# Kernel optimization log

Measured on AMD Instinct MI355X. Metric: run time of the kernel, lower is better.

## Reference

```python
import jax, jax.numpy as jnp
import numpy as np

QK = 32  # GGML Q8_0 block size

def dequant_q8_0(w_q, w_scales):
    # w_q: [out, in] int8-valued quants; w_scales: [out, in//QK] per-block scales
    out_f, in_f = w_q.shape
    q = w_q.astype(w_scales.dtype).reshape(out_f, in_f // QK, QK)
    w = q * w_scales[:, :, None]  # broadcast scale over block
    return w.reshape(out_f, in_f)

def setup_inputs() -> dict:
    key = jax.random.key(0)
    k1, k2, k3, k4 = jax.random.split(key, 4)
    OUT, IN, TOK = 12288, 3072, 4096
    x = jax.random.normal(k1, (TOK, IN), dtype=jnp.float32)
    w_q = jax.random.randint(k2, (OUT, IN), -127, 128, dtype=jnp.int32)
    w_scales = jax.random.uniform(k3, (OUT, IN // QK), dtype=jnp.float32) * 0.01
    bias = jax.random.normal(k4, (OUT,), dtype=jnp.float32) * 0.01
    return {"x": x, "w_q": w_q, "w_scales": w_scales, "bias": bias}

def reference(x, w_q, w_scales, bias):
    # DequantingLinear.forward: dequantize weight (and bias) then F.linear
    weight = dequant_q8_0(w_q, w_scales)          # [OUT, IN]
    return x @ weight.T + bias                    # [TOK, OUT]
```

## Files before the change

### kernel.cpp

```cpp
#include <hip/hip_runtime.h>
#include <hip/hip_bf16.h>
#include <stdint.h>


typedef __bf16 bf16;
typedef __bf16 bf16x8 __attribute__((ext_vector_type(8)));
typedef float f32x4 __attribute__((ext_vector_type(4)));

#define AS1 __attribute__((address_space(1)))
#define AS3 __attribute__((address_space(3)))

__device__ __forceinline__ void gload_lds16(const void* g, void* l) {
    __builtin_amdgcn_global_load_lds((AS1 void*)g, (AS3 void*)l, 16, 0, 0);
}

#define MFMA16(d, x, y) d = __builtin_amdgcn_mfma_f32_16x16x32_bf16(x, y, d, 0, 0, 0)

__global__ __launch_bounds__(128) void k_dequant(
    const int* __restrict__ q, const float* __restrict__ sc,
    bf16* __restrict__ w, int IN) {
    const int row = blockIdx.y;
    const int k = (blockIdx.x * 128 + threadIdx.x) * 8;
    if (k >= IN) return;
    const float s = sc[(size_t)row * (IN >> 5) + (k >> 5)];
    const size_t base = (size_t)row * IN + k;
    const int4 q0 = *(const int4*)(q + base);
    const int4 q1 = *(const int4*)(q + base + 4);
    bf16x8 o;
    o[0] = (bf16)(q0.x * s); o[1] = (bf16)(q0.y * s);
    o[2] = (bf16)(q0.z * s); o[3] = (bf16)(q0.w * s);
    o[4] = (bf16)(q1.x * s); o[5] = (bf16)(q1.y * s);
    o[6] = (bf16)(q1.z * s); o[7] = (bf16)(q1.w * s);
    *(bf16x8*)(w + base) = o;
}

__global__ __launch_bounds__(256) void k_cvt(
    const float* __restrict__ x, bf16* __restrict__ xb, long long n8) {
    long long i = (long long)blockIdx.x * 256 + threadIdx.x;
    const long long stride = (long long)gridDim.x * 256;
    for (; i < n8; i += stride) {
        const float4 a = *(const float4*)(x + i * 8);
        const float4 b = *(const float4*)(x + i * 8 + 4);
        bf16x8 o;
        o[0] = (bf16)a.x; o[1] = (bf16)a.y; o[2] = (bf16)a.z; o[3] = (bf16)a.w;
        o[4] = (bf16)b.x; o[5] = (bf16)b.y; o[6] = (bf16)b.z; o[7] = (bf16)b.w;
        *(bf16x8*)(xb + i * 8) = o;
    }
}

__global__ __launch_bounds__(512, 2) void k_gemm8p(
    const bf16* __restrict__ A, const bf16* __restrict__ B,
    const float* __restrict__ bias, float* __restrict__ C,
    int M, int N, int K) {
    __shared__ __align__(16) char lds[131072];
    const int tid = threadIdx.x;
    const int wv = tid >> 6, ln = tid & 63;
    const int wm = wv >> 2, wn = wv & 3;
    const int nbn = N >> 8;
    const int nwg = gridDim.x;
    const int q8 = nwg >> 3, r8 = nwg & 7;
    const int xcd = blockIdx.x & 7, lin = blockIdx.x >> 3;
    const int swz = (xcd < r8 ? xcd * (q8 + 1)
                              : r8 * (q8 + 1) + (xcd - r8) * q8) + lin;
    const int bm = swz / nbn, bn = swz % nbn;

    const size_t rowb = (size_t)K * 2;
    const int scol = (((tid ^ (tid >> 3)) & 7) << 4);
    const char* Ag = (const char*)A + ((size_t)(bm << 8) + (tid >> 3)) * rowb + scol;
    const char* Bg = (const char*)B + ((size_t)(bn << 8) + (tid >> 3)) * rowb + scol;
    const char* Ag128 = Ag + (size_t)128 * rowb;
    const char* Bg128 = Bg + (size_t)128 * rowb;
    const int ldsw = wv << 10;

#define STG(dst_, src_, kt_) do {                                             \
        const size_t kb_ = (size_t)(kt_) << 1;                                \
        gload_lds16((src_) + kb_, lds + (dst_) + ldsw);                       \
        gload_lds16((src_) + (size_t)64 * rowb + kb_,                         \
                    lds + (dst_) + 8192 + ldsw);                              \
    } while (0)

    const int colx = ((ln & 4) << 4) | ((((ln >> 4) ^ ln) & 3) << 4);
    const int c0 = colx, c1 = colx ^ 64;
    const int abase = (((wm << 7) + (ln & 15)) << 7);
    const int bbase = (((wn << 6) + (ln & 15)) << 7);

    f32x4 acc[8][4] = {};

#define SB __builtin_amdgcn_sched_barrier(0)
#define BAR __builtin_amdgcn_s_barrier()
#define VMW2 asm volatile("s_waitcnt vmcnt(2)" ::: "memory")
#define VMW0 asm volatile("s_waitcnt vmcnt(0)" ::: "memory")

#define PHASE(cb_, h_, c_, STAGE_STMT, ENDW_STMT) do {                        \
        const char* bA_ = lds + (cb_);                                        \
        const char* bB_ = lds + (cb_) + 32768;                                \
        bf16x8 paf[8], pbf[4];                                                \
        _Pragma("unroll")                                                     \
        for (int r = 0; r < 4; ++r) {                                         \
            paf[r*2+0] = *(const bf16x8*)(bA_ + abase + (h_)*8192 + (r<<11) + c0); \
            paf[r*2+1] = *(const bf16x8*)(bA_ + abase + (h_)*8192 + (r<<11) + c1); \
        }                                                                     \
        _Pragma("unroll")                                                     \
        for (int rb = 0; rb < 2; ++rb) {                                      \
            pbf[rb*2+0] = *(const bf16x8*)(bB_ + bbase + (((c_)*2+rb)<<11) + c0); \
            pbf[rb*2+1] = *(const bf16x8*)(bB_ + bbase + (((c_)*2+rb)<<11) + c1); \
        }                                                                     \
        STAGE_STMT;                                                           \
        SB; BAR; SB;                                                          \
        __builtin_amdgcn_s_setprio(1);                                        \
        _Pragma("unroll")                                                     \
        for (int r = 0; r < 4; ++r)                                           \
            _Pragma("unroll")                                                 \
            for (int rb = 0; rb < 2; ++rb) {                                  \
                MFMA16(acc[(h_)*4+r][(c_)*2+rb], paf[r*2+0], pbf[rb*2+0]);    \
                MFMA16(acc[(h_)*4+r][(c_)*2+rb], paf[r*2+1], pbf[rb*2+1]);    \
            }                                                                 \
        __builtin_amdgcn_s_setprio(0);                                        \
        ENDW_STMT;                                                            \
        SB; BAR; SB;                                                          \
    } while (0)

    STG(0,      Ag,    0);
    STG(16384,  Ag128, 0);
    STG(32768,  Bg,    0);
    STG(49152,  Bg128, 0);
    STG(65536,  Ag,    64);
    VMW2;
    SB; BAR; SB;

    const int NITER = K >> 7;
    for (int j = 0; j < NITER - 1; ++j) {
        const int kt1 = (j << 7) + 64, kt2 = kt1 + 64, kt3 = kt2 + 64;
        PHASE(0,     0, 0, STG(81920,  Ag128, kt1), (void)0);
        PHASE(0,     0, 1, STG(98304,  Bg,    kt1), (void)0);
        PHASE(0,     1, 0, STG(114688, Bg128, kt1), (void)0);
        PHASE(0,     1, 1, STG(0,      Ag,    kt2), VMW2);
        PHASE(65536, 0, 0, STG(16384,  Ag128, kt2), (void)0);
        PHASE(65536, 0, 1, STG(32768,  Bg,    kt2), (void)0);
        PHASE(65536, 1, 0, STG(49152,  Bg128, kt2), (void)0);
        PHASE(65536, 1, 1, STG(65536,  Ag,    kt3), VMW2);
    }
    {
        const int kt1 = ((NITER - 1) << 7) + 64;
        PHASE(0,     0, 0, STG(81920,  Ag128, kt1), (void)0);
        PHASE(0,     0, 1, STG(98304,  Bg,    kt1), (void)0);
        PHASE(0,     1, 0, STG(114688, Bg128, kt1), (void)0);
        PHASE(0,     1, 1, (void)0,                 VMW0);
        PHASE(65536, 0, 0, (void)0, (void)0);
        PHASE(65536, 0, 1, (void)0, (void)0);
        PHASE(65536, 1, 0, (void)0, (void)0);
        PHASE(65536, 1, 1, (void)0, (void)0);
    }
#undef PHASE
#undef STG

    const int erow = (bm << 8) + (wm << 7) + ((ln >> 4) << 2);
    const int ecol = (bn << 8) + (wn << 6) + (ln & 15);
    float bv[4];
#pragma unroll
    for (int n = 0; n < 4; ++n) bv[n] = bias[ecol + (n << 4)];
#pragma unroll
    for (int m = 0; m < 8; ++m)
#pragma unroll
        for (int r = 0; r < 4; ++r) {
            float* Crow = C + (size_t)(erow + (m << 4) + r) * N + ecol;
#pragma unroll
            for (int n = 0; n < 4; ++n)
                Crow[n << 4] = acc[m][n][r] + bv[n];
        }
}

__global__ __launch_bounds__(256) void k_fused(
    const float* __restrict__ X, const int* __restrict__ Q,
    const float* __restrict__ SC, const float* __restrict__ bias,
    float* __restrict__ C, int M, int N, int K) {
    __shared__ __align__(16) bf16 sA[128 * 32];
    __shared__ __align__(16) bf16 sB[128 * 32];
    const int tid = threadIdx.x;
    const int wv = tid >> 6;
    const int ln = tid & 63;
    const int nbn = N >> 7;
    const int nwg = gridDim.x;
    const int q8 = nwg >> 3, r8 = nwg & 7;
    const int xcd = blockIdx.x & 7, lin = blockIdx.x >> 3;
    const int swz = (xcd < r8 ? xcd * (q8 + 1)
                              : r8 * (q8 + 1) + (xcd - r8) * q8) + lin;
    const int bm = swz / nbn, bn = swz % nbn;
    const int wr = (wv >> 1) << 6;
    const int wc = (wv & 1) << 6;
    const int srow = tid >> 1;
    const int sk = (tid & 1) << 4;

    f32x4 acc[4][4] = {};
    const float* xrow = X + (size_t)((bm << 7) + srow) * K + sk;
    const int* qrow = Q + (size_t)((bn << 7) + srow) * K + sk;
    const float* scrow = SC + (size_t)((bn << 7) + srow) * (K >> 5);

    for (int kt = 0; kt < K; kt += 32) {
        const float4 a0 = *(const float4*)(xrow + kt);
        const float4 a1 = *(const float4*)(xrow + kt + 4);
        const float4 a2 = *(const float4*)(xrow + kt + 8);
        const float4 a3 = *(const float4*)(xrow + kt + 12);
        const int4 q0 = *(const int4*)(qrow + kt);
        const int4 q1 = *(const int4*)(qrow + kt + 4);
        const int4 q2 = *(const int4*)(qrow + kt + 8);
        const int4 q3 = *(const int4*)(qrow + kt + 12);
        const float s = scrow[(kt + sk) >> 5];
        bf16x8 wa0, wa1, wb0, wb1;
        wa0[0] = (bf16)a0.x; wa0[1] = (bf16)a0.y; wa0[2] = (bf16)a0.z; wa0[3] = (bf16)a0.w;
        wa0[4] = (bf16)a1.x; wa0[5] = (bf16)a1.y; wa0[6] = (bf16)a1.z; wa0[7] = (bf16)a1.w;
        wa1[0] = (bf16)a2.x; wa1[1] = (bf16)a2.y; wa1[2] = (bf16)a2.z; wa1[3] = (bf16)a2.w;
        wa1[4] = (bf16)a3.x; wa1[5] = (bf16)a3.y; wa1[6] = (bf16)a3.z; wa1[7] = (bf16)a3.w;
        wb0[0] = (bf16)(q0.x * s); wb0[1] = (bf16)(q0.y * s);
        wb0[2] = (bf16)(q0.z * s); wb0[3] = (bf16)(q0.w * s);
        wb0[4] = (bf16)(q1.x * s); wb0[5] = (bf16)(q1.y * s);
        wb0[6] = (bf16)(q1.z * s); wb0[7] = (bf16)(q1.w * s);
        wb1[0] = (bf16)(q2.x * s); wb1[1] = (bf16)(q2.y * s);
        wb1[2] = (bf16)(q2.z * s); wb1[3] = (bf16)(q2.w * s);
        wb1[4] = (bf16)(q3.x * s); wb1[5] = (bf16)(q3.y * s);
        wb1[6] = (bf16)(q3.z * s); wb1[7] = (bf16)(q3.w * s);
        __syncthreads();
        *(bf16x8*)(sA + srow * 32 + sk) = wa0;
        *(bf16x8*)(sA + srow * 32 + sk + 8) = wa1;
        *(bf16x8*)(sB + srow * 32 + sk) = wb0;
        *(bf16x8*)(sB + srow * 32 + sk + 8) = wb1;
        __syncthreads();

        bf16x8 af[4], bg[4];
#pragma unroll
        for (int m = 0; m < 4; ++m)
            af[m] = *(const bf16x8*)(sA + ((wr + (m << 4) + (ln & 15)) << 5) +
                                     ((ln >> 4) << 3));
#pragma unroll
        for (int n = 0; n < 4; ++n)
            bg[n] = *(const bf16x8*)(sB + ((wc + (n << 4) + (ln & 15)) << 5) +
                                     ((ln >> 4) << 3));
#pragma unroll
        for (int m = 0; m < 4; ++m)
#pragma unroll
            for (int n = 0; n < 4; ++n)
                acc[m][n] = __builtin_amdgcn_mfma_f32_16x16x32_bf16(
                    af[m], bg[n], acc[m][n], 0, 0, 0);
    }

    float bv[4];
#pragma unroll
    for (int n = 0; n < 4; ++n)
        bv[n] = bias[(bn << 7) + wc + (n << 4) + (ln & 15)];
#pragma unroll
    for (int m = 0; m < 4; ++m) {
        const int grow0 = (bm << 7) + wr + (m << 4) + ((ln >> 4) << 2);
#pragma unroll
        for (int r = 0; r < 4; ++r) {
            float* Crow = C + (size_t)(grow0 + r) * N;
#pragma unroll
            for (int n = 0; n < 4; ++n)
                Crow[(bn << 7) + wc + (n << 4) + (ln & 15)] =
                    acc[m][n][r] + bv[n];
        }
    }
}

extern "C" void kernel_launch(void* const* d_in, const int* in_sizes, int n_in,
                              void* d_out, int out_size, void* d_ws, size_t ws_size,
                              hipStream_t stream) {
    const float* x = (const float*)d_in[0];
    const int* wq = (const int*)d_in[1];
    const float* sc = (const float*)d_in[2];
    const float* bias = (const float*)d_in[3];
    float* out = (float*)d_out;

    const long long xN = in_sizes[0];
    const long long wN = in_sizes[1];
    const int OUT = in_sizes[3];
    const int IN = (int)(wN / OUT);
    const int TOK = (int)(xN / IN);
    const int M = TOK, N = OUT, K = IN;

    const size_t wb_bytes = (size_t)wN * 2;
    const size_t xb_bytes = (size_t)xN * 2;
    const bool ok8p = (M % 256 == 0) && (N % 256 == 0) && (K % 128 == 0) &&
                      (K >= 256);

    if (ok8p && ws_size >= wb_bytes + xb_bytes) {
        bf16* Wb = (bf16*)d_ws;
        bf16* Xb = (bf16*)((char*)d_ws + wb_bytes);
        dim3 dq_grid((IN / 8 + 127) / 128, OUT);
        k_dequant<<<dq_grid, 128, 0, stream>>>(wq, sc, Wb, IN);
        const long long n8 = xN / 8;
        int cvt_blocks = (int)((n8 + 255) / 256);
        if (cvt_blocks > 2048) cvt_blocks = 2048;
        k_cvt<<<cvt_blocks, 256, 0, stream>>>(x, Xb, n8);
        const int grid = (M / 256) * (N / 256);
        k_gemm8p<<<grid, 512, 0, stream>>>(Xb, Wb, bias, out, M, N, K);
    } else {
        const int grid = (M / 128) * (N / 128);
        k_fused<<<grid, 256, 0, stream>>>(x, wq, sc, bias, out, M, N, K);
    }
}
```

Baseline: 361.0 us.

## Restructure GEMM LDS staging into per-quadrant A/B loads with finer waits

Reorganizes the 8-phase bf16 MFMA GEMM pipeline so each phase stages one quadrant of A or B into the other double buffer. The previous one-stage-ahead ring offset is replaced by a plain two-buffer ping-pong. The B tile rows are remapped so each staged quadrant matches the column half consumed by a phase. Each phase now has one barrier plus a vmcnt(4) wait where the old code had two barriers per phase and vmcnt(2) waits. The aim is to reduce barrier overhead and keep more global loads in flight, at the cost of relying on subtle wait-count correctness. The K>=256 guard is also dropped.

```diff
diff --git a/kernel.cpp b/kernel.cpp
--- a/kernel.cpp
+++ b/kernel.cpp
@@ -67,46 +67,55 @@
     const size_t rowb = (size_t)K * 2;
     const int scol = (((tid ^ (tid >> 3)) & 7) << 4);
     const char* Ag = (const char*)A + ((size_t)(bm << 8) + (tid >> 3)) * rowb + scol;
-    const char* Bg = (const char*)B + ((size_t)(bn << 8) + (tid >> 3)) * rowb + scol;
-    const char* Ag128 = Ag + (size_t)128 * rowb;
-    const char* Bg128 = Bg + (size_t)128 * rowb;
+    const char* Bg = (const char*)B +
+        ((size_t)(bn << 8) + ((tid >> 8) << 6) + ((tid >> 3) & 31)) * rowb + scol;
     const int ldsw = wv << 10;
 
-#define STG(dst_, src_, kt_) do {                                             \
+#define STGA(bb_, h_, kt_) do {                                               \
         const size_t kb_ = (size_t)(kt_) << 1;                                \
-        gload_lds16((src_) + kb_, lds + (dst_) + ldsw);                       \
-        gload_lds16((src_) + (size_t)64 * rowb + kb_,                         \
-                    lds + (dst_) + 8192 + ldsw);                              \
+        gload_lds16(Ag + (size_t)((h_) << 6) * rowb + kb_,                    \
+                    lds + (bb_) + ((h_) << 14) + ldsw);                       \
+        gload_lds16(Ag + (size_t)(128 + ((h_) << 6)) * rowb + kb_,            \
+                    lds + (bb_) + ((h_) << 14) + 8192 + ldsw);                \
+    } while (0)
+#define STGB(bb_, c_, kt_) do {                                               \
+        const size_t kb_ = (size_t)(kt_) << 1;                                \
+        gload_lds16(Bg + (size_t)((c_) << 5) * rowb + kb_,                    \
+                    lds + (bb_) + 32768 + ((c_) << 14) + ldsw);               \
+        gload_lds16(Bg + (size_t)(128 + ((c_) << 5)) * rowb + kb_,            \
+                    lds + (bb_) + 32768 + ((c_) << 14) + 8192 + ldsw);        \
     } while (0)
 
     const int colx = ((ln & 4) << 4) | ((((ln >> 4) ^ ln) & 3) << 4);
     const int c0 = colx, c1 = colx ^ 64;
-    const int abase = (((wm << 7) + (ln & 15)) << 7);
-    const int bbase = (((wn << 6) + (ln & 15)) << 7);
+    const int arow = (wm << 13) + ((ln & 15) << 7);
+    const int brow = (wn << 12) + ((ln & 15) << 7);
 
     f32x4 acc[8][4] = {};
 
 #define SB __builtin_amdgcn_sched_barrier(0)
 #define BAR __builtin_amdgcn_s_barrier()
-#define VMW2 asm volatile("s_waitcnt vmcnt(2)" ::: "memory")
-#define VMW0 asm volatile("s_waitcnt vmcnt(0)" ::: "memory")
-
-#define PHASE(cb_, h_, c_, STAGE_STMT, ENDW_STMT) do {                        \
-        const char* bA_ = lds + (cb_);                                        \
-        const char* bB_ = lds + (cb_) + 32768;                                \
+#define EW4 do { asm volatile("s_waitcnt vmcnt(4)" ::: "memory"); SB; BAR; SB; } while (0)
+#define EW2 do { asm volatile("s_waitcnt vmcnt(2)" ::: "memory"); SB; BAR; SB; } while (0)
+#define EW0 do { asm volatile("s_waitcnt vmcnt(0)" ::: "memory"); SB; BAR; SB; } while (0)
+#define EWN do { BAR; SB; } while (0)
+
+#define PHASE(bb_, h_, c_, STAGE_STMT, ENDW_STMT) do {                        \
+        const char* uA_ = lds + (bb_) + ((h_) << 14);                         \
+        const char* uB_ = lds + (bb_) + 32768 + ((c_) << 14);                 \
         bf16x8 paf[8], pbf[4];                                                \
         _Pragma("unroll")                                                     \
         for (int r = 0; r < 4; ++r) {                                         \
-            paf[r*2+0] = *(const bf16x8*)(bA_ + abase + (h_)*8192 + (r<<11) + c0); \
-            paf[r*2+1] = *(const bf16x8*)(bA_ + abase + (h_)*8192 + (r<<11) + c1); \
+            paf[r*2+0] = *(const bf16x8*)(uA_ + arow + (r << 11) + c0);       \
+            paf[r*2+1] = *(const bf16x8*)(uA_ + arow + (r << 11) + c1);       \
         }                                                                     \
         _Pragma("unroll")                                                     \
         for (int rb = 0; rb < 2; ++rb) {                                      \
-            pbf[rb*2+0] = *(const bf16x8*)(bB_ + bbase + (((c_)*2+rb)<<11) + c0); \
-            pbf[rb*2+1] = *(const bf16x8*)(bB_ + bbase + (((c_)*2+rb)<<11) + c1); \
+            pbf[rb*2+0] = *(const bf16x8*)(uB_ + brow + (rb << 11) + c0);     \
+            pbf[rb*2+1] = *(const bf16x8*)(uB_ + brow + (rb << 11) + c1);     \
         }                                                                     \
         STAGE_STMT;                                                           \
-        SB; BAR; SB;                                                          \
+        BAR;                                                                  \
         __builtin_amdgcn_s_setprio(1);                                        \
         _Pragma("unroll")                                                     \
         for (int r = 0; r < 4; ++r)                                           \
@@ -117,42 +126,41 @@
             }                                                                 \
         __builtin_amdgcn_s_setprio(0);                                        \
         ENDW_STMT;                                                            \
-        SB; BAR; SB;                                                          \
     } while (0)
 
-    STG(0,      Ag,    0);
-    STG(16384,  Ag128, 0);
-    STG(32768,  Bg,    0);
-    STG(49152,  Bg128, 0);
-    STG(65536,  Ag,    64);
-    VMW2;
-    SB; BAR; SB;
+    STGA(0, 0, 0);
+    STGB(0, 0, 0);
+    STGB(0, 1, 0);
+    STGA(0, 1, 0);
+    EW4;
 
     const int NITER = K >> 7;
     for (int j = 0; j < NITER - 1; ++j) {
-        const int kt1 = (j << 7) + 64, kt2 = kt1 + 64, kt3 = kt2 + 64;
-        PHASE(0,     0, 0, STG(81920,  Ag128, kt1), (void)0);
-        PHASE(0,     0, 1, STG(98304,  Bg,    kt1), (void)0);
-        PHASE(0,     1, 0, STG(114688, Bg128, kt1), (void)0);
-        PHASE(0,     1, 1, STG(0,      Ag,    kt2), VMW2);
-        PHASE(65536, 0, 0, STG(16384,  Ag128, kt2), (void)0);
-        PHASE(65536, 0, 1, STG(32768,  Bg,    kt2), (void)0);
-        PHASE(65536, 1, 0, STG(49152,  Bg128, kt2), (void)0);
-        PHASE(65536, 1, 1, STG(65536,  Ag,    kt3), VMW2);
+        const int ko = (j << 7) + 64;
+        const int kn = (j << 7) + 128;
+        PHASE(0,     0, 0, STGA(65536, 0, ko), EW4);
+        PHASE(0,     0, 1, STGB(65536, 0, ko), EW4);
+        PHASE(0,     1, 1, STGB(65536, 1, ko), EWN);
+        PHASE(0,     1, 0, STGA(65536, 1, ko), EW4);
+        PHASE(65536, 0, 0, STGA(0, 0, kn),     EW4);
+        PHASE(65536, 0, 1, STGB(0, 0, kn),     EW4);
+        PHASE(65536, 1, 1, STGB(0, 1, kn),     EWN);
+        PHASE(65536, 1, 0, STGA(0, 1, kn),     EW4);
     }
     {
-        const int kt1 = ((NITER - 1) << 7) + 64;
-        PHASE(0,     0, 0, STG(81920,  Ag128, kt1), (void)0);
-        PHASE(0,     0, 1, STG(98304,  Bg,    kt1), (void)0);
-        PHASE(0,     1, 0, STG(114688, Bg128, kt1), (void)0);
-        PHASE(0,     1, 1, (void)0,                 VMW0);
-        PHASE(65536, 0, 0, (void)0, (void)0);
-        PHASE(65536, 0, 1, (void)0, (void)0);
-        PHASE(65536, 1, 0, (void)0, (void)0);
-        PHASE(65536, 1, 1, (void)0, (void)0);
+        const int ko = ((NITER - 1) << 7) + 64;
+        PHASE(0,     0, 0, STGA(65536, 0, ko), EW4);
+        PHASE(0,     0, 1, STGB(65536, 0, ko), EW4);
+        PHASE(0,     1, 1, STGB(65536, 1, ko), EWN);
+        PHASE(0,     1, 0, STGA(65536, 1, ko), EW4);
+        PHASE(65536, 0, 0, (void)0,            EW2);
+        PHASE(65536, 0, 1, (void)0,            EW0);
+        PHASE(65536, 1, 1, (void)0,            EWN);
+        PHASE(65536, 1, 0, (void)0,            EWN);
     }
 #undef PHASE
-#undef STG
+#undef STGA
+#undef STGB
 
     const int erow = (bm << 8) + (wm << 7) + ((ln >> 4) << 2);
     const int ecol = (bn << 8) + (wn << 6) + (ln & 15);
@@ -279,8 +287,7 @@
 
     const size_t wb_bytes = (size_t)wN * 2;
     const size_t xb_bytes = (size_t)xN * 2;
-    const bool ok8p = (M % 256 == 0) && (N % 256 == 0) && (K % 128 == 0) &&
-                      (K >= 256);
+    const bool ok8p = (M % 256 == 0) && (N % 256 == 0) && (K % 128 == 0);
 
     if (ok8p && ws_size >= wb_bytes + xb_bytes) {
         bf16* Wb = (bf16*)d_ws;
```

Measured after the change: 361.9 us. No clear change (+0.2%).

## Reuse LDS fragments across MFMA clusters with serpentine order and reworked staging

Applied to the files above, without the earlier changes.

Reorders the 8-phase GEMM main loop into a serpentine cluster order (h0c0, h0c1, h1c1, h1c0) so A and B register fragments read from LDS are reused across consecutive MFMA clusters instead of reloaded every phase. This cuts LDS read traffic per K-step. The global-to-LDS staging schedule and buffer slot assignments are also reworked, with the waitcnt changed to vmcnt(4) and the sched_barrier hints removed. The changes add register pressure from keeping two B fragment sets live, and they risk new hazards in the reworked LDS buffer reuse ordering.

```diff
diff --git a/kernel.cpp b/kernel.cpp
--- a/kernel.cpp
+++ b/kernel.cpp
@@ -65,94 +65,101 @@
     const int bm = swz / nbn, bn = swz % nbn;
 
     const size_t rowb = (size_t)K * 2;
+    const size_t r64 = (size_t)64 * rowb, r128 = (size_t)128 * rowb;
     const int scol = (((tid ^ (tid >> 3)) & 7) << 4);
     const char* Ag = (const char*)A + ((size_t)(bm << 8) + (tid >> 3)) * rowb + scol;
     const char* Bg = (const char*)B + ((size_t)(bn << 8) + (tid >> 3)) * rowb + scol;
-    const char* Ag128 = Ag + (size_t)128 * rowb;
-    const char* Bg128 = Bg + (size_t)128 * rowb;
+    const char* Ah = Ag + r128;
+    const char* Bh = Bg + r128;
     const int ldsw = wv << 10;
 
-#define STG(dst_, src_, kt_) do {                                             \
+#define STGU(bb_, uo_, src_, kt_) do {                                        \
         const size_t kb_ = (size_t)(kt_) << 1;                                \
-        gload_lds16((src_) + kb_, lds + (dst_) + ldsw);                       \
-        gload_lds16((src_) + (size_t)64 * rowb + kb_,                         \
-                    lds + (dst_) + 8192 + ldsw);                              \
+        gload_lds16((src_) + kb_, lds + (bb_) + (uo_) + ldsw);                \
+        gload_lds16((src_) + r64 + kb_, lds + (bb_) + (uo_) + 8192 + ldsw);   \
     } while (0)
 
-    const int colx = ((ln & 4) << 4) | ((((ln >> 4) ^ ln) & 3) << 4);
-    const int c0 = colx, c1 = colx ^ 64;
-    const int abase = (((wm << 7) + (ln & 15)) << 7);
-    const int bbase = (((wn << 6) + (ln & 15)) << 7);
+    const int c0 = ((ln & 4) << 4) | ((((ln >> 4) ^ ln) & 3) << 4);
+    const int c1 = c0 ^ 64;
+    const int arow = ((wm << 7) + (ln & 15)) << 7;
+    const int brow = 32768 + (((wn << 6) + (ln & 15)) << 7);
 
     f32x4 acc[8][4] = {};
-
-#define SB __builtin_amdgcn_sched_barrier(0)
+    bf16x8 pa[8], pb0[4], pb1[4];
+
+#define RDA(bb_, h_) do { _Pragma("unroll")                                   \
+        for (int mm = 0; mm < 4; ++mm) {                                      \
+            pa[mm*2+0] = *(const bf16x8*)(lds + (bb_) + arow + (h_)*8192 + mm*2048 + c0); \
+            pa[mm*2+1] = *(const bf16x8*)(lds + (bb_) + arow + (h_)*8192 + mm*2048 + c1); \
+        } } while (0)
+#define RDB(bb_, c_, PB_) do { _Pragma("unroll")                              \
+        for (int nn = 0; nn < 2; ++nn) {                                      \
+            PB_[nn*2+0] = *(const bf16x8*)(lds + (bb_) + brow + ((c_)*2+nn)*2048 + c0); \
+            PB_[nn*2+1] = *(const bf16x8*)(lds + (bb_) + brow + ((c_)*2+nn)*2048 + c1); \
+        } } while (0)
+#define CLUSTER(h_, c_, PB_) do {                                             \
+        __builtin_amdgcn_s_setprio(1);                                        \
+        _Pragma("unroll") for (int ks = 0; ks < 2; ++ks)                      \
+            _Pragma("unroll") for (int mm = 0; mm < 4; ++mm)                  \
+                _Pragma("unroll") for (int nn = 0; nn < 2; ++nn)              \
+                    MFMA16(acc[(h_)*4+mm][(c_)*2+nn], pa[mm*2+ks], PB_[nn*2+ks]); \
+        __builtin_amdgcn_s_setprio(0);                                        \
+    } while (0)
+
 #define BAR __builtin_amdgcn_s_barrier()
-#define VMW2 asm volatile("s_waitcnt vmcnt(2)" ::: "memory")
+#define VMW4 asm volatile("s_waitcnt vmcnt(4)" ::: "memory")
 #define VMW0 asm volatile("s_waitcnt vmcnt(0)" ::: "memory")
 
-#define PHASE(cb_, h_, c_, STAGE_STMT, ENDW_STMT) do {                        \
-        const char* bA_ = lds + (cb_);                                        \
-        const char* bB_ = lds + (cb_) + 32768;                                \
-        bf16x8 paf[8], pbf[4];                                                \
-        _Pragma("unroll")                                                     \
-        for (int r = 0; r < 4; ++r) {                                         \
-            paf[r*2+0] = *(const bf16x8*)(bA_ + abase + (h_)*8192 + (r<<11) + c0); \
-            paf[r*2+1] = *(const bf16x8*)(bA_ + abase + (h_)*8192 + (r<<11) + c1); \
-        }                                                                     \
-        _Pragma("unroll")                                                     \
-        for (int rb = 0; rb < 2; ++rb) {                                      \
-            pbf[rb*2+0] = *(const bf16x8*)(bB_ + bbase + (((c_)*2+rb)<<11) + c0); \
-            pbf[rb*2+1] = *(const bf16x8*)(bB_ + bbase + (((c_)*2+rb)<<11) + c1); \
-        }                                                                     \
-        STAGE_STMT;                                                           \
-        SB; BAR; SB;                                                          \
-        __builtin_amdgcn_s_setprio(1);                                        \
-        _Pragma("unroll")                                                     \
-        for (int r = 0; r < 4; ++r)                                           \
-            _Pragma("unroll")                                                 \
-            for (int rb = 0; rb < 2; ++rb) {                                  \
-                MFMA16(acc[(h_)*4+r][(c_)*2+rb], paf[r*2+0], pbf[rb*2+0]);    \
-                MFMA16(acc[(h_)*4+r][(c_)*2+rb], paf[r*2+1], pbf[rb*2+1]);    \
-            }                                                                 \
-        __builtin_amdgcn_s_setprio(0);                                        \
-        ENDW_STMT;                                                            \
-        SB; BAR; SB;                                                          \
-    } while (0)
-
-    STG(0,      Ag,    0);
-    STG(16384,  Ag128, 0);
-    STG(32768,  Bg,    0);
-    STG(49152,  Bg128, 0);
-    STG(65536,  Ag,    64);
-    VMW2;
-    SB; BAR; SB;
-
-    const int NITER = K >> 7;
-    for (int j = 0; j < NITER - 1; ++j) {
-        const int kt1 = (j << 7) + 64, kt2 = kt1 + 64, kt3 = kt2 + 64;
-        PHASE(0,     0, 0, STG(81920,  Ag128, kt1), (void)0);
-        PHASE(0,     0, 1, STG(98304,  Bg,    kt1), (void)0);
-        PHASE(0,     1, 0, STG(114688, Bg128, kt1), (void)0);
-        PHASE(0,     1, 1, STG(0,      Ag,    kt2), VMW2);
-        PHASE(65536, 0, 0, STG(16384,  Ag128, kt2), (void)0);
-        PHASE(65536, 0, 1, STG(32768,  Bg,    kt2), (void)0);
-        PHASE(65536, 1, 0, STG(49152,  Bg128, kt2), (void)0);
-        PHASE(65536, 1, 1, STG(65536,  Ag,    kt3), VMW2);
+    STGU(0, 0,     Ag, 0);
+    STGU(0, 16384, Ah, 0);
+    STGU(0, 32768, Bg, 0);
+    STGU(0, 49152, Bh, 0);
+    STGU(65536, 32768, Bg, 64);
+    STGU(65536, 49152, Bh, 64);
+    VMW4;
+    BAR;
+
+    const int NI = K >> 7;
+    for (int j = 0; j < NI - 1; ++j) {
+        const int kT1 = (j << 7) + 64, kT2 = kT1 + 64, kT3 = kT2 + 64;
+        RDA(0, 0); RDB(0, 0, pb0); STGU(65536, 0, Ag, kT1);
+        BAR; CLUSTER(0, 0, pb0); BAR;
+        RDB(0, 1, pb1); STGU(65536, 16384, Ah, kT1);
+        BAR; CLUSTER(0, 1, pb1); BAR;
+        RDA(0, 1); STGU(0, 32768, Bg, kT2);
+        BAR; CLUSTER(1, 1, pb1); BAR;
+        STGU(0, 49152, Bh, kT2);
+        BAR; CLUSTER(1, 0, pb0); VMW4; BAR;
+        RDA(65536, 0); RDB(65536, 0, pb0); STGU(0, 0, Ag, kT2);
+        BAR; CLUSTER(0, 0, pb0); BAR;
+        RDB(65536, 1, pb1); STGU(0, 16384, Ah, kT2);
+        BAR; CLUSTER(0, 1, pb1); BAR;
+        RDA(65536, 1); STGU(65536, 32768, Bg, kT3);
+        BAR; CLUSTER(1, 1, pb1); BAR;
+        STGU(65536, 49152, Bh, kT3);
+        BAR; CLUSTER(1, 0, pb0); VMW4; BAR;
     }
     {
-        const int kt1 = ((NITER - 1) << 7) + 64;
-        PHASE(0,     0, 0, STG(81920,  Ag128, kt1), (void)0);
-        PHASE(0,     0, 1, STG(98304,  Bg,    kt1), (void)0);
-        PHASE(0,     1, 0, STG(114688, Bg128, kt1), (void)0);
-        PHASE(0,     1, 1, (void)0,                 VMW0);
-        PHASE(65536, 0, 0, (void)0, (void)0);
-        PHASE(65536, 0, 1, (void)0, (void)0);
-        PHASE(65536, 1, 0, (void)0, (void)0);
-        PHASE(65536, 1, 1, (void)0, (void)0);
-    }
-#undef PHASE
-#undef STG
+        const int kT1 = ((NI - 1) << 7) + 64;
+        RDA(0, 0); RDB(0, 0, pb0); STGU(65536, 0, Ag, kT1);
+        BAR; CLUSTER(0, 0, pb0); BAR;
+        RDB(0, 1, pb1); STGU(65536, 16384, Ah, kT1);
+        BAR; CLUSTER(0, 1, pb1); BAR;
+        RDA(0, 1);
+        BAR; CLUSTER(1, 1, pb1); BAR;
+        BAR; CLUSTER(1, 0, pb0); VMW0; BAR;
+        RDA(65536, 0); RDB(65536, 0, pb0);
+        BAR; CLUSTER(0, 0, pb0); BAR;
+        RDB(65536, 1, pb1);
+        BAR; CLUSTER(0, 1, pb1); BAR;
+        RDA(65536, 1);
+        BAR; CLUSTER(1, 1, pb1); BAR;
+        BAR; CLUSTER(1, 0, pb0); BAR;
+    }
+#undef STGU
+#undef RDA
+#undef RDB
+#undef CLUSTER
 
     const int erow = (bm << 8) + (wm << 7) + ((ln >> 4) << 2);
     const int ecol = (bn << 8) + (wn << 6) + (ln & 15);
```

Measured after the change: 332.8 us. 1.08x faster.

## Restructure GEMM LDS layout into 32-wide K sub-slices with B-fragment reuse

Applied to the files above, without the earlier changes.

The LDS staging layout changes so that each 64-wide K tile is split into two 32-wide K sub-slices, each laid out with a new XOR swizzle. Each phase now reads 4 A fragments and, on alternate phases only, 4 B fragments, and issues one MFMA per accumulator instead of two. The aim is fewer LDS reads per MFMA and fewer bank conflicts. In exchange, the load-issue ordering and vmcnt waits are reworked, which makes the pipeline more fragile, and the sched_barriers are removed in favour of an explicit lgkmcnt wait.

```diff
diff --git a/kernel.cpp b/kernel.cpp
--- a/kernel.cpp
+++ b/kernel.cpp
@@ -65,91 +65,94 @@
     const int bm = swz / nbn, bn = swz % nbn;
 
     const size_t rowb = (size_t)K * 2;
-    const int scol = (((tid ^ (tid >> 3)) & 7) << 4);
-    const char* Ag = (const char*)A + ((size_t)(bm << 8) + (tid >> 3)) * rowb + scol;
-    const char* Bg = (const char*)B + ((size_t)(bn << 8) + (tid >> 3)) * rowb + scol;
-    const char* Ag128 = Ag + (size_t)128 * rowb;
-    const char* Bg128 = Bg + (size_t)128 * rowb;
+    const int L0 = tid, L1 = tid + 512;
+    const int x0 = (L0 & 7) ^ ((L0 >> 3) & 7);
+    const int x1 = (L1 & 7) ^ ((L1 >> 3) & 7);
+    const int fr0 = ((L0 >> 3) << 1) | (x0 >> 2), c40 = x0 & 3;
+    const int fr1 = ((L1 >> 3) << 1) | (x1 >> 2), c41 = x1 & 3;
+    const char* Asrc0 = (const char*)A + ((size_t)(bm << 8) + fr0) * rowb + c40 * 16;
+    const char* Asrc1 = (const char*)A + ((size_t)(bm << 8) + fr1) * rowb + c41 * 16;
+    const char* Bsrc0 = (const char*)B + ((size_t)(bn << 8) + fr0) * rowb + c40 * 16;
+    const char* Bsrc1 = (const char*)B + ((size_t)(bn << 8) + fr1) * rowb + c41 * 16;
     const int ldsw = wv << 10;
 
-#define STG(dst_, src_, kt_) do {                                             \
+#define STG(bb_, uo_, kt_, P_) do {                                           \
         const size_t kb_ = (size_t)(kt_) << 1;                                \
-        gload_lds16((src_) + kb_, lds + (dst_) + ldsw);                       \
-        gload_lds16((src_) + (size_t)64 * rowb + kb_,                         \
-                    lds + (dst_) + 8192 + ldsw);                              \
+        gload_lds16(P_##src0 + kb_, lds + (bb_) + (uo_) + ldsw);              \
+        gload_lds16(P_##src1 + kb_, lds + (bb_) + (uo_) + 8192 + ldsw);       \
     } while (0)
 
-    const int colx = ((ln & 4) << 4) | ((((ln >> 4) ^ ln) & 3) << 4);
-    const int c0 = colx, c1 = colx ^ 64;
-    const int abase = (((wm << 7) + (ln & 15)) << 7);
-    const int bbase = (((wn << 6) + (ln & 15)) << 7);
+    const int chunk = (((ln & 1) << 2) | (ln >> 4)) ^ ((ln >> 1) & 7);
+    const int aoff = (wm << 13) + (((ln & 15) >> 1) << 7) + (chunk << 4);
+    const int boff = (wn << 12) + (((ln & 15) >> 1) << 7) + (chunk << 4);
 
     f32x4 acc[8][4] = {};
-
-#define SB __builtin_amdgcn_sched_barrier(0)
+    bf16x8 pb[4];
+
 #define BAR __builtin_amdgcn_s_barrier()
-#define VMW2 asm volatile("s_waitcnt vmcnt(2)" ::: "memory")
+#define VMW6 asm volatile("s_waitcnt vmcnt(6)" ::: "memory")
 #define VMW0 asm volatile("s_waitcnt vmcnt(0)" ::: "memory")
-
-#define PHASE(cb_, h_, c_, STAGE_STMT, ENDW_STMT) do {                        \
-        const char* bA_ = lds + (cb_);                                        \
-        const char* bB_ = lds + (cb_) + 32768;                                \
-        bf16x8 paf[8], pbf[4];                                                \
+#define NOST (void)0
+
+#define PHASE(bb_, h_, ks_, RDB_, STAGE_STMT, ENDW_STMT) do {                 \
+        const char* base_ = lds + (bb_) + (ks_) * 16384;                      \
+        bf16x8 pa_[4];                                                        \
         _Pragma("unroll")                                                     \
-        for (int r = 0; r < 4; ++r) {                                         \
-            paf[r*2+0] = *(const bf16x8*)(bA_ + abase + (h_)*8192 + (r<<11) + c0); \
-            paf[r*2+1] = *(const bf16x8*)(bA_ + abase + (h_)*8192 + (r<<11) + c1); \
-        }                                                                     \
-        _Pragma("unroll")                                                     \
-        for (int rb = 0; rb < 2; ++rb) {                                      \
-            pbf[rb*2+0] = *(const bf16x8*)(bB_ + bbase + (((c_)*2+rb)<<11) + c0); \
-            pbf[rb*2+1] = *(const bf16x8*)(bB_ + bbase + (((c_)*2+rb)<<11) + c1); \
+        for (int m = 0; m < 4; ++m)                                           \
+            pa_[m] = *(const bf16x8*)(base_ + ((h_) << 12) + aoff + (m << 10)); \
+        if (RDB_) {                                                           \
+            _Pragma("unroll")                                                 \
+            for (int n = 0; n < 4; ++n)                                       \
+                pb[n] = *(const bf16x8*)(base_ + 32768 + boff + (n << 10));   \
         }                                                                     \
         STAGE_STMT;                                                           \
-        SB; BAR; SB;                                                          \
+        BAR;                                                                  \
+        asm volatile("s_waitcnt lgkmcnt(0)" ::: "memory");                    \
         __builtin_amdgcn_s_setprio(1);                                        \
         _Pragma("unroll")                                                     \
-        for (int r = 0; r < 4; ++r)                                           \
+        for (int m = 0; m < 4; ++m)                                           \
             _Pragma("unroll")                                                 \
-            for (int rb = 0; rb < 2; ++rb) {                                  \
-                MFMA16(acc[(h_)*4+r][(c_)*2+rb], paf[r*2+0], pbf[rb*2+0]);    \
-                MFMA16(acc[(h_)*4+r][(c_)*2+rb], paf[r*2+1], pbf[rb*2+1]);    \
-            }                                                                 \
+            for (int n = 0; n < 4; ++n)                                       \
+                MFMA16(acc[(h_) * 4 + m][n], pa_[m], pb[n]);                  \
         __builtin_amdgcn_s_setprio(0);                                        \
         ENDW_STMT;                                                            \
-        SB; BAR; SB;                                                          \
+        BAR;                                                                  \
     } while (0)
 
-    STG(0,      Ag,    0);
-    STG(16384,  Ag128, 0);
-    STG(32768,  Bg,    0);
-    STG(49152,  Bg128, 0);
-    STG(65536,  Ag,    64);
-    VMW2;
-    SB; BAR; SB;
-
-    const int NITER = K >> 7;
-    for (int j = 0; j < NITER - 1; ++j) {
-        const int kt1 = (j << 7) + 64, kt2 = kt1 + 64, kt3 = kt2 + 64;
-        PHASE(0,     0, 0, STG(81920,  Ag128, kt1), (void)0);
-        PHASE(0,     0, 1, STG(98304,  Bg,    kt1), (void)0);
-        PHASE(0,     1, 0, STG(114688, Bg128, kt1), (void)0);
-        PHASE(0,     1, 1, STG(0,      Ag,    kt2), VMW2);
-        PHASE(65536, 0, 0, STG(16384,  Ag128, kt2), (void)0);
-        PHASE(65536, 0, 1, STG(32768,  Bg,    kt2), (void)0);
-        PHASE(65536, 1, 0, STG(49152,  Bg128, kt2), (void)0);
-        PHASE(65536, 1, 1, STG(65536,  Ag,    kt3), VMW2);
+    STG(0, 0,     0,  A);
+    STG(0, 16384, 32, A);
+    STG(0, 32768, 0,  B);
+    STG(0, 49152, 32, B);
+    STG(65536, 32768, 64, B);
+    STG(65536, 0,     64, A);
+    STG(65536, 49152, 96, B);
+    VMW6;
+    BAR;
+
+    const int NI = K >> 7;
+    for (int j = 0; j < NI - 1; ++j) {
+        const int kO = (j << 7) + 64;
+        const int kE = (j << 7) + 128;
+        const int kN = (j << 7) + 192;
+        PHASE(0,     0, 0, 1, STG(65536, 16384, kO + 32, A), NOST);
+        PHASE(0,     1, 0, 0, STG(0,     32768, kE,      B), NOST);
+        PHASE(0,     0, 1, 1, STG(0,     0,     kE,      A), NOST);
+        PHASE(0,     1, 1, 0, STG(0,     49152, kE + 32, B), VMW6);
+        PHASE(65536, 0, 0, 1, STG(0,     16384, kE + 32, A), NOST);
+        PHASE(65536, 1, 0, 0, STG(65536, 32768, kN,      B), NOST);
+        PHASE(65536, 0, 1, 1, STG(65536, 0,     kN,      A), NOST);
+        PHASE(65536, 1, 1, 0, STG(65536, 49152, kN + 32, B), VMW6);
     }
     {
-        const int kt1 = ((NITER - 1) << 7) + 64;
-        PHASE(0,     0, 0, STG(81920,  Ag128, kt1), (void)0);
-        PHASE(0,     0, 1, STG(98304,  Bg,    kt1), (void)0);
-        PHASE(0,     1, 0, STG(114688, Bg128, kt1), (void)0);
-        PHASE(0,     1, 1, (void)0,                 VMW0);
-        PHASE(65536, 0, 0, (void)0, (void)0);
-        PHASE(65536, 0, 1, (void)0, (void)0);
-        PHASE(65536, 1, 0, (void)0, (void)0);
-        PHASE(65536, 1, 1, (void)0, (void)0);
+        const int kO = ((NI - 1) << 7) + 64;
+        PHASE(0,     0, 0, 1, STG(65536, 16384, kO + 32, A), NOST);
+        PHASE(0,     1, 0, 0, NOST,                          NOST);
+        PHASE(0,     0, 1, 1, NOST,                          NOST);
+        PHASE(0,     1, 1, 0, NOST,                          VMW0);
+        PHASE(65536, 0, 0, 1, NOST,                          NOST);
+        PHASE(65536, 1, 0, 0, NOST,                          NOST);
+        PHASE(65536, 0, 1, 1, NOST,                          NOST);
+        PHASE(65536, 1, 1, 0, NOST,                          NOST);
     }
 #undef PHASE
 #undef STG
```

After: 342.8 us. 1.05x faster.
